# Performance work log

Hardware: AMD Instinct MI355X
Metric: run time of the kernel (lower is better)

Reference implementation:

```python
import jax, jax.numpy as jnp
import numpy as np

D, B, E, O = 16, 8, 2048, 2048  # delays, batch, pre, post


def setup_inputs() -> dict:
    key = jax.random.key(0)
    k1, k2, k3, k4, k5, k6 = jax.random.split(key, 6)
    # Sparse nonnegative connectivity scaled by wmax (here wmax=1)
    conn = (jax.random.uniform(k1, (E, O)) < 0.2).astype(jnp.float32)
    W = jax.random.uniform(k2, (E, O), dtype=jnp.float32) * conn
    # align_signs: per-presynaptic-neuron sign in {-1,+1}, zeroed where W<=0
    signs_pre = jnp.where(jax.random.uniform(k3, (E,)) < 0.8, 1.0, -1.0)
    signs = jnp.where(W > 0, signs_pre[:, None], 0.0).astype(jnp.float32)
    Xd = (jax.random.uniform(k4, (D, B, E)) < 0.05).astype(jnp.float32)
    # STP module output (before the +1 applied in forward)
    Wshort = 0.1 * jax.random.normal(k5, (D, B, E), dtype=jnp.float32)
    # delaymap: binary routing mask (delay, pre, post)
    delaymap = (jax.random.uniform(k6, (D, E, O)) < 0.3).astype(jnp.float32)
    return {"W": W, "signs": signs, "Xd": Xd, "Wshort": Wshort, "delaymap": delaymap}


def reference(W, signs, Xd, Wshort, delaymap):
    # DeltaSynapse.forward, active, has_STDP=False, has_STP=True:
    #   W_eff = signs * W                      (e, o)
    #   Wshort_mod = shortterm(Xd) + 1         (d, b, e)
    #   I = einsum('eo,dbe,deo,dbe->bo', W_eff, Xd, delaymap, Wshort_mod)
    Weff = signs * W
    I = jnp.einsum('eo,dbe,deo,dbe->bo', Weff, Xd, delaymap, Wshort + 1.0)
    return I
```

## Files before the change

kernel.cpp:

```cpp
#include <hip/hip_runtime.h>
#include <cstdint>
#include <cstddef>

#define DD 16
#define BB 8
#define EE 2048
#define OO 2048

__global__ void pack_coeffs(const float* __restrict__ Xd,
                            const float* __restrict__ Ws,
                            float* __restrict__ Cpack) {
    int i = blockIdx.x * 256 + threadIdx.x;
    if (i >= DD * BB * EE) return;
    int e  = i & (EE - 1);
    int db = i >> 11;
    int d  = db >> 3;
    int b  = db & 7;
    float x = Xd[i];
    float v = x * (Ws[i] + 1.0f);
    Cpack[((size_t)e * DD + d) * BB + b] = v;
}

__global__ void build_mask(const float* __restrict__ Cpack,
                           unsigned* __restrict__ mask) {
    int e = blockIdx.x * 256 + threadIdx.x;
    if (e >= EE) return;
    const float4* c4 = reinterpret_cast<const float4*>(Cpack + (size_t)e * DD * BB);
    unsigned m = 0;
    for (int d = 0; d < DD; ++d) {
        float4 a = c4[d * 2];
        float4 b = c4[d * 2 + 1];
        bool nz = (a.x != 0.f) | (a.y != 0.f) | (a.z != 0.f) | (a.w != 0.f) |
                  (b.x != 0.f) | (b.y != 0.f) | (b.z != 0.f) | (b.w != 0.f);
        m |= (nz ? 1u : 0u) << d;
    }
    mask[e] = m;
}

__device__ __forceinline__ void fma4(float4& a, const float4& x, float s) {
    a.x = fmaf(x.x, s, a.x);
    a.y = fmaf(x.y, s, a.y);
    a.z = fmaf(x.z, s, a.z);
    a.w = fmaf(x.w, s, a.w);
}

template <bool USE_PACK, bool USE_PART>
__global__ __launch_bounds__(256, 2)
void synapse_main(const float* __restrict__ W,
                  const float* __restrict__ S,
                  const float* __restrict__ Xd,
                  const float* __restrict__ Ws,
                  const float* __restrict__ DM,
                  const float* __restrict__ Cpack,
                  const unsigned* __restrict__ mask,
                  float* __restrict__ Pout) {
    const int ot   = blockIdx.x;
    const int ch   = blockIdx.y;
    const int wave = threadIdx.x >> 6;
    const int lane = threadIdx.x & 63;
    const int o0   = ot * 256 + lane * 4;
    const int e_begin = ch * 32 + wave * 8;

    float4 acc[BB];
#pragma unroll
    for (int b = 0; b < BB; ++b) acc[b] = make_float4(0.f, 0.f, 0.f, 0.f);

    for (int ei = 0; ei < 8; ++ei) {
        const int e = e_begin + ei;

        float4 w4 = *reinterpret_cast<const float4*>(W + (size_t)e * OO + o0);
        float4 s4 = *reinterpret_cast<const float4*>(S + (size_t)e * OO + o0);
        float4 wf;
        wf.x = w4.x * s4.x; wf.y = w4.y * s4.y;
        wf.z = w4.z * s4.z; wf.w = w4.w * s4.w;

        if (USE_PACK) {
            unsigned m = mask[e];
            while (m) {
                const int d = __builtin_ctz(m);
                m &= (m - 1);
                const float4* cp = reinterpret_cast<const float4*>(
                    Cpack + ((size_t)e * DD + d) * BB);
                float4 c0 = cp[0];
                float4 c1 = cp[1];
                float4 dm = *reinterpret_cast<const float4*>(
                    DM + ((size_t)d * EE + e) * OO + o0);
                float4 dw;
                dw.x = dm.x * wf.x; dw.y = dm.y * wf.y;
                dw.z = dm.z * wf.z; dw.w = dm.w * wf.w;
                fma4(acc[0], dw, c0.x); fma4(acc[1], dw, c0.y);
                fma4(acc[2], dw, c0.z); fma4(acc[3], dw, c0.w);
                fma4(acc[4], dw, c1.x); fma4(acc[5], dw, c1.y);
                fma4(acc[6], dw, c1.z); fma4(acc[7], dw, c1.w);
            }
        } else {
            for (int d = 0; d < DD; ++d) {
                float c[BB];
                bool nz = false;
#pragma unroll
                for (int b = 0; b < BB; ++b) {
                    size_t idx = (size_t)(d * BB + b) * EE + e;
                    float x = Xd[idx];
                    c[b] = x * (Ws[idx] + 1.0f);
                    nz |= (c[b] != 0.f);
                }
                if (!nz) continue;
                float4 dm = *reinterpret_cast<const float4*>(
                    DM + ((size_t)d * EE + e) * OO + o0);
                float4 dw;
                dw.x = dm.x * wf.x; dw.y = dm.y * wf.y;
                dw.z = dm.z * wf.z; dw.w = dm.w * wf.w;
#pragma unroll
                for (int b = 0; b < BB; ++b) fma4(acc[b], dw, c[b]);
            }
        }
    }

    if (USE_PART) {
        __shared__ __align__(16) float red[4][BB][256];
#pragma unroll
        for (int b = 0; b < BB; ++b)
            *reinterpret_cast<float4*>(&red[wave][b][lane * 4]) = acc[b];
        __syncthreads();
        const int t = threadIdx.x;
#pragma unroll
        for (int b = 0; b < BB; ++b) {
            float s = red[0][b][t] + red[1][b][t] + red[2][b][t] + red[3][b][t];
            Pout[((size_t)ch * BB + b) * OO + ot * 256 + t] = s;
        }
    } else {
#pragma unroll
        for (int b = 0; b < BB; ++b) {
            float* op = Pout + (size_t)b * OO + o0;
            atomicAdd(op + 0, acc[b].x);
            atomicAdd(op + 1, acc[b].y);
            atomicAdd(op + 2, acc[b].z);
            atomicAdd(op + 3, acc[b].w);
        }
    }
}

__global__ void reduce_partials(const float* __restrict__ P,
                                float* __restrict__ out) {
    int i = blockIdx.x * 256 + threadIdx.x;
    if (i >= BB * OO) return;
    int b = i >> 11;
    int o = i & (OO - 1);
    float s = 0.f;
    for (int ch = 0; ch < 64; ++ch)
        s += P[((size_t)ch * BB + b) * OO + o];
    out[(size_t)b * OO + o] = s;
}

extern "C" void kernel_launch(void* const* d_in, const int* in_sizes, int n_in,
                              void* d_out, int out_size, void* d_ws, size_t ws_size,
                              hipStream_t stream) {
    const float* W  = (const float*)d_in[0];
    const float* S  = (const float*)d_in[1];
    const float* Xd = (const float*)d_in[2];
    const float* Ws = (const float*)d_in[3];
    const float* DM = (const float*)d_in[4];
    float* out = (float*)d_out;

    const size_t packBytes = (size_t)EE * DD * BB * sizeof(float);
    const size_t maskBytes = (size_t)EE * sizeof(unsigned);
    const size_t partBytes = (size_t)64 * BB * OO * sizeof(float);

    char* ws = (char*)d_ws;
    const bool canPack = ws_size >= packBytes + maskBytes;
    const bool canPart = ws_size >= packBytes + maskBytes + partBytes;

    dim3 grid(8, 64), blk(256);

    if (canPart) {
        float*    Cp = (float*)ws;
        unsigned* mk = (unsigned*)(ws + packBytes);
        float*    P  = (float*)(ws + packBytes + maskBytes);
        pack_coeffs<<<(DD * BB * EE + 255) / 256, 256, 0, stream>>>(Xd, Ws, Cp);
        build_mask<<<(EE + 255) / 256, 256, 0, stream>>>(Cp, mk);
        synapse_main<true, true><<<grid, blk, 0, stream>>>(W, S, Xd, Ws, DM, Cp, mk, P);
        reduce_partials<<<(BB * OO + 255) / 256, 256, 0, stream>>>(P, out);
    } else if (canPack) {
        float*    Cp = (float*)ws;
        unsigned* mk = (unsigned*)(ws + packBytes);
        hipMemsetAsync(out, 0, (size_t)BB * OO * sizeof(float), stream);
        pack_coeffs<<<(DD * BB * EE + 255) / 256, 256, 0, stream>>>(Xd, Ws, Cp);
        build_mask<<<(EE + 255) / 256, 256, 0, stream>>>(Cp, mk);
        synapse_main<true, false><<<grid, blk, 0, stream>>>(W, S, Xd, Ws, DM, Cp, mk, out);
    } else {
        hipMemsetAsync(out, 0, (size_t)BB * OO * sizeof(float), stream);
        synapse_main<false, false><<<grid, blk, 0, stream>>>(W, S, Xd, Ws, DM,
                                                             nullptr, nullptr, out);
    }
}
```

Before: 367.0 us.

## Split E into more chunks, raise occupancy, fold mask build into pack kernel

Raises the number of E-chunks from 64 to 256, so each wave handles 2 presynaptic rows instead of 8. The grid grows to 2048 blocks, and launch bounds are raised to 6 blocks per CU to increase memory parallelism for the delaymap-bound stream. The mask is now built with atomicOr inside pack_coeffs, which removes one kernel launch. The LDS reduction is halved by doing two passes of four batches, and reduce_partials is unrolled with four accumulators. The cost is four times more partial-sum traffic and a heavier final reduction, plus extra atomics in pack.

```diff
diff --git a/kernel.cpp b/kernel.cpp
--- a/kernel.cpp
+++ b/kernel.cpp
@@ -6,10 +6,12 @@
 #define BB 8
 #define EE 2048
 #define OO 2048
+#define NCH 256
 
 __global__ void pack_coeffs(const float* __restrict__ Xd,
                             const float* __restrict__ Ws,
-                            float* __restrict__ Cpack) {
+                            float* __restrict__ Cpack,
+                            unsigned* __restrict__ mask) {
     int i = blockIdx.x * 256 + threadIdx.x;
     if (i >= DD * BB * EE) return;
     int e  = i & (EE - 1);
@@ -19,22 +21,7 @@
     float x = Xd[i];
     float v = x * (Ws[i] + 1.0f);
     Cpack[((size_t)e * DD + d) * BB + b] = v;
-}
-
-__global__ void build_mask(const float* __restrict__ Cpack,
-                           unsigned* __restrict__ mask) {
-    int e = blockIdx.x * 256 + threadIdx.x;
-    if (e >= EE) return;
-    const float4* c4 = reinterpret_cast<const float4*>(Cpack + (size_t)e * DD * BB);
-    unsigned m = 0;
-    for (int d = 0; d < DD; ++d) {
-        float4 a = c4[d * 2];
-        float4 b = c4[d * 2 + 1];
-        bool nz = (a.x != 0.f) | (a.y != 0.f) | (a.z != 0.f) | (a.w != 0.f) |
-                  (b.x != 0.f) | (b.y != 0.f) | (b.z != 0.f) | (b.w != 0.f);
-        m |= (nz ? 1u : 0u) << d;
-    }
-    mask[e] = m;
+    if (v != 0.0f) atomicOr(&mask[e], 1u << d);
 }
 
 __device__ __forceinline__ void fma4(float4& a, const float4& x, float s) {
@@ -44,12 +31,10 @@
     a.w = fmaf(x.w, s, a.w);
 }
 
-template <bool USE_PACK, bool USE_PART>
-__global__ __launch_bounds__(256, 2)
+template <bool USE_PART>
+__global__ __launch_bounds__(256, 6)
 void synapse_main(const float* __restrict__ W,
                   const float* __restrict__ S,
-                  const float* __restrict__ Xd,
-                  const float* __restrict__ Ws,
                   const float* __restrict__ DM,
                   const float* __restrict__ Cpack,
                   const unsigned* __restrict__ mask,
@@ -59,14 +44,14 @@
     const int wave = threadIdx.x >> 6;
     const int lane = threadIdx.x & 63;
     const int o0   = ot * 256 + lane * 4;
-    const int e_begin = ch * 32 + wave * 8;
 
     float4 acc[BB];
 #pragma unroll
     for (int b = 0; b < BB; ++b) acc[b] = make_float4(0.f, 0.f, 0.f, 0.f);
 
-    for (int ei = 0; ei < 8; ++ei) {
-        const int e = e_begin + ei;
+#pragma unroll
+    for (int ei = 0; ei < 2; ++ei) {
+        const int e = ch * 8 + wave * 2 + ei;
 
         float4 w4 = *reinterpret_cast<const float4*>(W + (size_t)e * OO + o0);
         float4 s4 = *reinterpret_cast<const float4*>(S + (size_t)e * OO + o0);
@@ -74,69 +59,50 @@
         wf.x = w4.x * s4.x; wf.y = w4.y * s4.y;
         wf.z = w4.z * s4.z; wf.w = w4.w * s4.w;
 
-        if (USE_PACK) {
-            unsigned m = mask[e];
-            while (m) {
-                const int d = __builtin_ctz(m);
-                m &= (m - 1);
-                const float4* cp = reinterpret_cast<const float4*>(
-                    Cpack + ((size_t)e * DD + d) * BB);
-                float4 c0 = cp[0];
-                float4 c1 = cp[1];
-                float4 dm = *reinterpret_cast<const float4*>(
-                    DM + ((size_t)d * EE + e) * OO + o0);
-                float4 dw;
-                dw.x = dm.x * wf.x; dw.y = dm.y * wf.y;
-                dw.z = dm.z * wf.z; dw.w = dm.w * wf.w;
-                fma4(acc[0], dw, c0.x); fma4(acc[1], dw, c0.y);
-                fma4(acc[2], dw, c0.z); fma4(acc[3], dw, c0.w);
-                fma4(acc[4], dw, c1.x); fma4(acc[5], dw, c1.y);
-                fma4(acc[6], dw, c1.z); fma4(acc[7], dw, c1.w);
+        unsigned m = mask[e];
+        while (m) {
+            const int d = __builtin_ctz(m);
+            m &= (m - 1);
+            const float4* cp = reinterpret_cast<const float4*>(
+                Cpack + ((size_t)e * DD + d) * BB);
+            float4 c0 = cp[0];
+            float4 c1 = cp[1];
+            float4 dm = *reinterpret_cast<const float4*>(
+                DM + ((size_t)d * EE + e) * OO + o0);
+            float4 dw;
+            dw.x = dm.x * wf.x; dw.y = dm.y * wf.y;
+            dw.z = dm.z * wf.z; dw.w = dm.w * wf.w;
+            fma4(acc[0], dw, c0.x); fma4(acc[1], dw, c0.y);
+            fma4(acc[2], dw, c0.z); fma4(acc[3], dw, c0.w);
+            fma4(acc[4], dw, c1.x); fma4(acc[5], dw, c1.y);
+            fma4(acc[6], dw, c1.z); fma4(acc[7], dw, c1.w);
+        }
+    }
+
+    __shared__ __align__(16) float red[4][4][256];
+    const int t = threadIdx.x;
+#pragma unroll
+    for (int p = 0; p < 2; ++p) {
+#pragma unroll
+        for (int bb = 0; bb < 4; ++bb)
+            *reinterpret_cast<float4*>(&red[wave][bb][lane * 4]) = acc[p * 4 + bb];
+        __syncthreads();
+        if (USE_PART) {
+#pragma unroll
+            for (int bb = 0; bb < 4; ++bb) {
+                float s = red[0][bb][t] + red[1][bb][t] +
+                          red[2][bb][t] + red[3][bb][t];
+                Pout[((size_t)ch * BB + (p * 4 + bb)) * OO + ot * 256 + t] = s;
             }
         } else {
-            for (int d = 0; d < DD; ++d) {
-                float c[BB];
-                bool nz = false;
-#pragma unroll
-                for (int b = 0; b < BB; ++b) {
-                    size_t idx = (size_t)(d * BB + b) * EE + e;
-                    float x = Xd[idx];
-                    c[b] = x * (Ws[idx] + 1.0f);
-                    nz |= (c[b] != 0.f);
-                }
-                if (!nz) continue;
-                float4 dm = *reinterpret_cast<const float4*>(
-                    DM + ((size_t)d * EE + e) * OO + o0);
-                float4 dw;
-                dw.x = dm.x * wf.x; dw.y = dm.y * wf.y;
-                dw.z = dm.z * wf.z; dw.w = dm.w * wf.w;
-#pragma unroll
-                for (int b = 0; b < BB; ++b) fma4(acc[b], dw, c[b]);
+#pragma unroll
+            for (int bb = 0; bb < 4; ++bb) {
+                float s = red[0][bb][t] + red[1][bb][t] +
+                          red[2][bb][t] + red[3][bb][t];
+                atomicAdd(Pout + (size_t)(p * 4 + bb) * OO + ot * 256 + t, s);
             }
         }
-    }
-
-    if (USE_PART) {
-        __shared__ __align__(16) float red[4][BB][256];
-#pragma unroll
-        for (int b = 0; b < BB; ++b)
-            *reinterpret_cast<float4*>(&red[wave][b][lane * 4]) = acc[b];
-        __syncthreads();
-        const int t = threadIdx.x;
-#pragma unroll
-        for (int b = 0; b < BB; ++b) {
-            float s = red[0][b][t] + red[1][b][t] + red[2][b][t] + red[3][b][t];
-            Pout[((size_t)ch * BB + b) * OO + ot * 256 + t] = s;
-        }
-    } else {
-#pragma unroll
-        for (int b = 0; b < BB; ++b) {
-            float* op = Pout + (size_t)b * OO + o0;
-            atomicAdd(op + 0, acc[b].x);
-            atomicAdd(op + 1, acc[b].y);
-            atomicAdd(op + 2, acc[b].z);
-            atomicAdd(op + 3, acc[b].w);
-        }
+        __syncthreads();
     }
 }
 
@@ -146,10 +112,82 @@
     if (i >= BB * OO) return;
     int b = i >> 11;
     int o = i & (OO - 1);
-    float s = 0.f;
-    for (int ch = 0; ch < 64; ++ch)
-        s += P[((size_t)ch * BB + b) * OO + o];
-    out[(size_t)b * OO + o] = s;
+    float s0 = 0.f, s1 = 0.f, s2 = 0.f, s3 = 0.f;
+    const float* p = P + (size_t)b * OO + o;
+#pragma unroll 4
+    for (int ch = 0; ch < NCH; ch += 4) {
+        s0 += p[(size_t)(ch + 0) * BB * OO];
+        s1 += p[(size_t)(ch + 1) * BB * OO];
+        s2 += p[(size_t)(ch + 2) * BB * OO];
+        s3 += p[(size_t)(ch + 3) * BB * OO];
+    }
+    out[(size_t)b * OO + o] = (s0 + s1) + (s2 + s3);
+}
+
+__global__ __launch_bounds__(256, 6)
+void synapse_nows(const float* __restrict__ W,
+                  const float* __restrict__ S,
+                  const float* __restrict__ Xd,
+                  const float* __restrict__ Ws,
+                  const float* __restrict__ DM,
+                  float* __restrict__ out) {
+    const int ot   = blockIdx.x;
+    const int ch   = blockIdx.y;
+    const int wave = threadIdx.x >> 6;
+    const int lane = threadIdx.x & 63;
+    const int o0   = ot * 256 + lane * 4;
+
+    float4 acc[BB];
+#pragma unroll
+    for (int b = 0; b < BB; ++b) acc[b] = make_float4(0.f, 0.f, 0.f, 0.f);
+
+#pragma unroll
+    for (int ei = 0; ei < 2; ++ei) {
+        const int e = ch * 8 + wave * 2 + ei;
+
+        float4 w4 = *reinterpret_cast<const float4*>(W + (size_t)e * OO + o0);
+        float4 s4 = *reinterpret_cast<const float4*>(S + (size_t)e * OO + o0);
+        float4 wf;
+        wf.x = w4.x * s4.x; wf.y = w4.y * s4.y;
+        wf.z = w4.z * s4.z; wf.w = w4.w * s4.w;
+
+        for (int d = 0; d < DD; ++d) {
+            float c[BB];
+            bool nz = false;
+#pragma unroll
+            for (int b = 0; b < BB; ++b) {
+                size_t idx = (size_t)(d * BB + b) * EE + e;
+                float x = Xd[idx];
+                c[b] = x * (Ws[idx] + 1.0f);
+                nz |= (c[b] != 0.f);
+            }
+            if (!nz) continue;
+            float4 dm = *reinterpret_cast<const float4*>(
+                DM + ((size_t)d * EE + e) * OO + o0);
+            float4 dw;
+            dw.x = dm.x * wf.x; dw.y = dm.y * wf.y;
+            dw.z = dm.z * wf.z; dw.w = dm.w * wf.w;
+#pragma unroll
+            for (int b = 0; b < BB; ++b) fma4(acc[b], dw, c[b]);
+        }
+    }
+
+    __shared__ __align__(16) float red[4][4][256];
+    const int t = threadIdx.x;
+#pragma unroll
+    for (int p = 0; p < 2; ++p) {
+#pragma unroll
+        for (int bb = 0; bb < 4; ++bb)
+            *reinterpret_cast<float4*>(&red[wave][bb][lane * 4]) = acc[p * 4 + bb];
+        __syncthreads();
+#pragma unroll
+        for (int bb = 0; bb < 4; ++bb) {
+            float s = red[0][bb][t] + red[1][bb][t] +
+                      red[2][bb][t] + red[3][bb][t];
+            atomicAdd(out + (size_t)(p * 4 + bb) * OO + ot * 256 + t, s);
+        }
+        __syncthreads();
+    }
 }
 
 extern "C" void kernel_launch(void* const* d_in, const int* in_sizes, int n_in,
@@ -164,32 +202,29 @@
 
     const size_t packBytes = (size_t)EE * DD * BB * sizeof(float);
     const size_t maskBytes = (size_t)EE * sizeof(unsigned);
-    const size_t partBytes = (size_t)64 * BB * OO * sizeof(float);
+    const size_t partBytes = (size_t)NCH * BB * OO * sizeof(float);
 
     char* ws = (char*)d_ws;
     const bool canPack = ws_size >= packBytes + maskBytes;
     const bool canPart = ws_size >= packBytes + maskBytes + partBytes;
 
-    dim3 grid(8, 64), blk(256);
-
-    if (canPart) {
+    dim3 grid(8, NCH), blk(256);
+
+    if (canPack) {
         float*    Cp = (float*)ws;
         unsigned* mk = (unsigned*)(ws + packBytes);
-        float*    P  = (float*)(ws + packBytes + maskBytes);
-        pack_coeffs<<<(DD * BB * EE + 255) / 256, 256, 0, stream>>>(Xd, Ws, Cp);
-        build_mask<<<(EE + 255) / 256, 256, 0, stream>>>(Cp, mk);
-        synapse_main<true, true><<<grid, blk, 0, stream>>>(W, S, Xd, Ws, DM, Cp, mk, P);
-        reduce_partials<<<(BB * OO + 255) / 256, 256, 0, stream>>>(P, out);
-    } else if (canPack) {
-        float*    Cp = (float*)ws;
-        unsigned* mk = (unsigned*)(ws + packBytes);
-        hipMemsetAsync(out, 0, (size_t)BB * OO * sizeof(float), stream);
-        pack_coeffs<<<(DD * BB * EE + 255) / 256, 256, 0, stream>>>(Xd, Ws, Cp);
-        build_mask<<<(EE + 255) / 256, 256, 0, stream>>>(Cp, mk);
-        synapse_main<true, false><<<grid, blk, 0, stream>>>(W, S, Xd, Ws, DM, Cp, mk, out);
+        hipMemsetAsync(mk, 0, maskBytes, stream);
+        pack_coeffs<<<(DD * BB * EE + 255) / 256, 256, 0, stream>>>(Xd, Ws, Cp, mk);
+        if (canPart) {
+            float* P = (float*)(ws + packBytes + maskBytes);
+            synapse_main<true><<<grid, blk, 0, stream>>>(W, S, DM, Cp, mk, P);
+            reduce_partials<<<(BB * OO + 255) / 256, 256, 0, stream>>>(P, out);
+        } else {
+            hipMemsetAsync(out, 0, (size_t)BB * OO * sizeof(float), stream);
+            synapse_main<false><<<grid, blk, 0, stream>>>(W, S, DM, Cp, mk, out);
+        }
     } else {
         hipMemsetAsync(out, 0, (size_t)BB * OO * sizeof(float), stream);
-        synapse_main<false, false><<<grid, blk, 0, stream>>>(W, S, Xd, Ws, DM,
-                                                             nullptr, nullptr, out);
-    }
-}
+        synapse_nows<<<grid, blk, 0, stream>>>(W, S, Xd, Ws, DM, out);
+    }
+}
```

New measurement: 377.7 us. 1.03x slower.
